# Optimization experiments

Measured on AMD Instinct MI355X. Metric: run time of the kernel, lower is better.

## Reference

```python
import jax, jax.numpy as jnp
import numpy as np


def setup_inputs() -> dict:
    key = jax.random.key(0)
    k1, k2 = jax.random.split(key)
    x = jax.random.normal(k1, (16, 128, 64, 64), dtype=jnp.float32)
    # weight layout: [out_channels, in_channels, kh, kw], kernel must be 3 for the
    # original Python-loop bounds to match the allocated output size
    weight = jax.random.normal(k2, (256, 128, 3, 3), dtype=jnp.float32) * 0.05
    return {"x": x, "weight": weight}


def reference(x, weight):
    # Stride-1 conv2d with symmetric zero padding=1 (forward ignores bias/stride/
    # dilation/groups in the original module).
    pad = 1
    out = jax.lax.conv_general_dilated(
        x, weight,
        window_strides=(1, 1),
        padding=[(pad, pad), (pad, pad)],
        dimension_numbers=("NCHW", "OIHW", "NCHW"),
    )
    return out
```

## Files before the change

### kernel.cpp

```cpp
#include <hip/hip_runtime.h>
#include <hip/hip_bf16.h>
#include <stdint.h>

typedef short bf16x8 __attribute__((ext_vector_type(8)));
typedef float f32x16 __attribute__((ext_vector_type(16)));

#define N_IMG 16
#define C_IN  128
#define H_IMG 64
#define W_IMG 64
#define K_OUT 256

#define XB_BYTES (16ull*66*66*128*2)
#define WB_BYTES (9ull*256*128*2)
#define WS_NEED  (XB_BYTES + WB_BYTES)

#define LDSX_BYTES (6*66*256)
#define WCH_BYTES  16384
#define LDS_TOTAL  (LDSX_BYTES + 3*WCH_BYTES)

__device__ __forceinline__ void gload16(void* lds, const void* g) {
    __builtin_amdgcn_global_load_lds(
        (const __attribute__((address_space(1))) void*)g,
        (__attribute__((address_space(3))) void*)lds, 16, 0, 0);
}

__device__ __forceinline__ uint32_t pack2(float a, float b) {
    __hip_bfloat16 ha = __float2bfloat16(a), hb = __float2bfloat16(b);
    return (uint32_t)*(uint16_t*)&ha | ((uint32_t)*(uint16_t*)&hb << 16);
}

__global__ __launch_bounds__(256)
void transform_fused_kernel(const float* __restrict__ x, const float* __restrict__ w,
                            __hip_bfloat16* __restrict__ xb, __hip_bfloat16* __restrict__ wb) {
    __shared__ __align__(16) uint32_t xs[64 * 64];
    const int b = blockIdx.x;
    const int t = threadIdx.x;

    if (b < 1056) {
        const int yt = b % 66;
        const int n  = b / 66;
        const bool interior = (yt >= 1 && yt <= 64);

        if (interior) {
            const float4* src = (const float4*)(x + (size_t)n * 524288 + (size_t)(yt - 1) * 64);
            #pragma unroll
            for (int it = 0; it < 4; ++it) {
                const int x4 = t & 15;
                const int j  = (t >> 4) + it * 16;
                float4 va = src[(2 * j) * 1024 + x4];
                float4 vb = src[(2 * j + 1) * 1024 + x4];
                const float* pa = (const float*)&va;
                const float* pb = (const float*)&vb;
                #pragma unroll
                for (int i = 0; i < 4; ++i) {
                    int row = x4 * 4 + i;
                    xs[row * 64 + (j ^ (((row >> 2) & 3) << 2))] = pack2(pa[i], pb[i]);
                }
            }
        }
        __syncthreads();

        uint4* dst = (uint4*)((char*)xb + (size_t)(n * 66 + yt) * 66 * 256);
        #pragma unroll
        for (int it = 0; it < 5; ++it) {
            int ch = t + it * 256;
            if (ch < 1056) {
                int xt = ch >> 4, u = ch & 15;
                uint4 val = make_uint4(0u, 0u, 0u, 0u);
                if (interior && xt >= 1 && xt <= 64) {
                    int row = xt - 1;
                    val = *(const uint4*)&xs[row * 64 + 4 * (u ^ ((row >> 2) & 3))];
                }
                dst[ch] = val;
            }
        }
    } else {
        const int kg = b - 1056;
        #pragma unroll
        for (int it = 0; it < 5; ++it) {
            int e = t + it * 256;
            if (e < 1152) {
                int tap = e >> 7;
                int c   = e & 127;
                wb[(tap * 256 + kg) * 128 + c] =
                    __float2bfloat16(w[kg * 1152 + c * 9 + tap]);
            }
        }
    }
}

__global__ __launch_bounds__(512, 2)
void conv3x3_mfma_kernel(const char* __restrict__ xg,
                         const char* __restrict__ wg,
                         float* __restrict__ out) {
    __shared__ uint4 smem[LDS_TOTAL / 16];
    char* lds  = (char*)smem;
    char* ldsW = lds + LDSX_BYTES;

    const int t    = threadIdx.x;
    const int b    = blockIdx.x;
    const int q    = b & 15;
    const int n    = b >> 4;
    const int lane = t & 63;
    const int wv   = t >> 6;
    const int lm   = lane & 31;
    const int hi   = lane >> 5;
    const int kb   = (wv >> 1) * 64;
    const int mb   = (wv & 1) * 128;

    int addrW[2][2];
    #pragma unroll
    for (int kf = 0; kf < 2; ++kf) {
        int krow = kb + kf * 32 + lm;
        #pragma unroll
        for (int ks = 0; ks < 2; ++ks)
            addrW[kf][ks] = krow * 64 + ((ks * 32 + hi * 16) ^ ((krow & 3) << 4));
    }
    int rc0[4];
    #pragma unroll
    for (int f = 0; f < 4; ++f) {
        int m = mb + f * 32 + lm;
        rc0[f] = (m >> 6) * 66 + (m & 63);
    }

    const int krow0 = t >> 2;
    const int woffA = krow0 * 256 + (((t & 3) ^ (krow0 & 3)) << 4);

    const char* xsrc = xg + (size_t)(n * 66 + q * 4) * 66 * 256;
    for (int ch = t; ch < 6336; ch += 512) {
        int L = ch * 16;
        gload16(lds + L, xsrc + (L ^ (((L >> 8) & 7) << 4)));
    }
    #pragma unroll
    for (int jj = 0; jj < 2; ++jj) {
        const char* s = wg + (jj >> 2) * 65536 + (jj & 3) * 64;
        char* d = ldsW + jj * WCH_BYTES + t * 16;
        gload16(d, s + woffA);
        gload16(d + 8192, s + woffA + 32768);
    }
    asm volatile("s_waitcnt vmcnt(2)" ::: "memory");
    __builtin_amdgcn_sched_barrier(0);
    __builtin_amdgcn_s_barrier();

    f32x16 acc[2][4];
    #pragma unroll
    for (int i = 0; i < 2; ++i)
        #pragma unroll
        for (int j = 0; j < 4; ++j)
            acc[i][j] = (f32x16)(0.f);

    int bR = 0;
    int bP = 2;

    auto loadx = [&](bf16x8 (&X)[2][4], int jj) {
        int tap = jj >> 2, cc = jj & 3;
        int r   = (tap >= 6) ? 2 : (tap >= 3 ? 1 : 0);
        int s_  = tap - r * 3;
        int rs66 = r * 66 + s_;
        #pragma unroll
        for (int ks = 0; ks < 2; ++ks) {
            const int co = cc * 64 + ks * 32 + hi * 16;
            #pragma unroll
            for (int f = 0; f < 4; ++f) {
                int rc = rc0[f] + rs66;
                int L  = rc * 256 + (co ^ ((rc & 7) << 4));
                X[ks][f] = *(const bf16x8*)(lds + L);
            }
        }
    };

    auto chunk = [&](int j, bf16x8 (&XC)[2][4], bf16x8 (&XN)[2][4]) {
        int jj2 = j + 2; if (jj2 >= 36) jj2 -= 36;
        {
            int tap2 = jj2 >> 2, cc2 = jj2 & 3;
            const char* s = wg + tap2 * 65536 + cc2 * 64;
            char* d = ldsW + bP * WCH_BYTES + t * 16;
            gload16(d, s + woffA);
            gload16(d + 8192, s + woffA + 32768);
        }
        const char* wbuf = ldsW + bR * WCH_BYTES;
        bf16x8 a[2][2];
        #pragma unroll
        for (int kf = 0; kf < 2; ++kf)
            #pragma unroll
            for (int ks = 0; ks < 2; ++ks)
                a[kf][ks] = *(const bf16x8*)(wbuf + addrW[kf][ks]);
        int jn = j + 1; if (jn >= 36) jn -= 36;
        loadx(XN, jn);

        __builtin_amdgcn_s_setprio(1);
        #pragma unroll
        for (int ks = 0; ks < 2; ++ks) {
            #pragma unroll
            for (int f = 0; f < 4; ++f) {
                acc[0][f] = __builtin_amdgcn_mfma_f32_32x32x16_bf16(a[0][ks], XC[ks][f], acc[0][f], 0, 0, 0);
                acc[1][f] = __builtin_amdgcn_mfma_f32_32x32x16_bf16(a[1][ks], XC[ks][f], acc[1][f], 0, 0, 0);
            }
        }
        __builtin_amdgcn_s_setprio(0);

        asm volatile("s_waitcnt vmcnt(2)" ::: "memory");
        __builtin_amdgcn_sched_barrier(0);
        __builtin_amdgcn_s_barrier();

        bR = (bR == 2) ? 0 : bR + 1;
        bP = (bP == 2) ? 0 : bP + 1;
    };

    bf16x8 xA[2][4], xB[2][4];
    loadx(xA, 0);
    for (int j = 0; j < 36; j += 2) {
        chunk(j,     xA, xB);
        chunk(j + 1, xB, xA);
    }

    const int y0 = q * 4;
    #pragma unroll
    for (int kf = 0; kf < 2; ++kf) {
        const int kbase2 = kb + kf * 32 + 4 * hi;
        #pragma unroll
        for (int f = 0; f < 4; ++f) {
            int m  = mb + f * 32 + lm;
            int yy = m >> 6;
            int xx = m & 63;
            float* op = out + (((size_t)(n * 256 + kbase2) * 64) + y0 + yy) * 64 + xx;
            #pragma unroll
            for (int reg = 0; reg < 16; ++reg) {
                int koff = (reg & 3) + 8 * (reg >> 2);
                op[(size_t)koff * 4096] = acc[kf][f][reg];
            }
        }
    }
}

__global__ __launch_bounds__(256, 3)
void conv3x3_f32_kernel(const float* __restrict__ x,
                        const float* __restrict__ w,
                        float* __restrict__ out) {
    __shared__ float xs[16][3][72];
    __shared__ float ws[16][9][64];

    const int t  = threadIdx.x;
    const int kt = blockIdx.x & 3;
    const int y  = (blockIdx.x >> 2) & 63;
    const int n  = blockIdx.x >> 8;

    const int k2   = t >> 3;
    const int xg   = t & 7;
    const int kloc = k2 * 2;
    const int x0   = xg * 8;

    float acc0[8] = {0.f,0.f,0.f,0.f,0.f,0.f,0.f,0.f};
    float acc1[8] = {0.f,0.f,0.f,0.f,0.f,0.f,0.f,0.f};

    const int k0 = kt * 64;

    for (int c0 = 0; c0 < C_IN; c0 += 16) {
        for (int idx = t; idx < 16 * 3 * 66; idx += 256) {
            int col = idx % 66;
            int rc  = idx / 66;
            int r   = rc % 3;
            int c   = rc / 3;
            int gx  = col - 1;
            int gy  = y - 1 + r;
            float v = 0.f;
            if ((unsigned)gx < (unsigned)W_IMG && (unsigned)gy < (unsigned)H_IMG)
                v = x[(((n * C_IN) + c0 + c) * H_IMG + gy) * W_IMG + gx];
            xs[c][r][col] = v;
        }
        for (int idx = t; idx < 64 * 16 * 9; idx += 256) {
            int tap = idx % 9;
            int ck  = idx / 9;
            int c   = ck % 16;
            int k   = ck / 16;
            ws[c][tap][k] = w[((k0 + k) * C_IN + c0 + c) * 9 + tap];
        }
        __syncthreads();

        #pragma unroll 2
        for (int c = 0; c < 16; ++c) {
            #pragma unroll
            for (int r = 0; r < 3; ++r) {
                float xr[10];
                #pragma unroll
                for (int i = 0; i < 10; ++i) xr[i] = xs[c][r][x0 + i];
                #pragma unroll
                for (int s = 0; s < 3; ++s) {
                    float w0 = ws[c][r * 3 + s][kloc];
                    float w1 = ws[c][r * 3 + s][kloc + 1];
                    #pragma unroll
                    for (int i = 0; i < 8; ++i) {
                        acc0[i] = fmaf(w0, xr[i + s], acc0[i]);
                        acc1[i] = fmaf(w1, xr[i + s], acc1[i]);
                    }
                }
            }
        }
        __syncthreads();
    }

    float* o0 = &out[(((n * K_OUT) + k0 + kloc) * H_IMG + y) * W_IMG + x0];
    float* o1 = o0 + H_IMG * W_IMG;
    #pragma unroll
    for (int i = 0; i < 8; ++i) o0[i] = acc0[i];
    #pragma unroll
    for (int i = 0; i < 8; ++i) o1[i] = acc1[i];
}

extern "C" void kernel_launch(void* const* d_in, const int* in_sizes, int n_in,
                              void* d_out, int out_size, void* d_ws, size_t ws_size,
                              hipStream_t stream) {
    const float* x = (const float*)d_in[0];
    const float* w = (const float*)d_in[1];
    float* out = (float*)d_out;
    (void)in_sizes; (void)n_in; (void)out_size;

    if (ws_size >= WS_NEED) {
        __hip_bfloat16* xb = (__hip_bfloat16*)d_ws;
        __hip_bfloat16* wb = (__hip_bfloat16*)((char*)d_ws + XB_BYTES);
        transform_fused_kernel<<<1056 + 256, 256, 0, stream>>>(x, w, xb, wb);
        conv3x3_mfma_kernel<<<256, 512, 0, stream>>>((const char*)xb, (const char*)wb, out);
    } else {
        conv3x3_f32_kernel<<<4096, 256, 0, stream>>>(x, w, out);
    }
}
```

Baseline: 132.9 us.

## Load conv weights directly from global into registers, drop LDS weight buffering

The weight transform now writes a pre-swizzled, MFMA-fragment-ordered layout, so each lane can load its A operands straight from global memory with contiguous 16-byte reads. The conv kernel drops the triple-buffered LDS weight staging and the per-chunk block barriers, and prefetches weight fragments two chunks ahead into registers. X fragment loads are restructured into a macro-unrolled per-tap loop with precomputed addresses. The aim is to remove LDS traffic and synchronization for weights, at the cost of more registers and exposing global/L2 latency on the weight loads.

After: 127.3 us. -4.2%, faster.

```diff
diff --git a/kernel.cpp b/kernel.cpp
--- a/kernel.cpp
+++ b/kernel.cpp
@@ -12,12 +12,10 @@
 #define K_OUT 256
 
 #define XB_BYTES (16ull*66*66*128*2)
-#define WB_BYTES (9ull*256*128*2)
+#define WB_BYTES (36ull*8*2*64*16)
 #define WS_NEED  (XB_BYTES + WB_BYTES)
 
 #define LDSX_BYTES (6*66*256)
-#define WCH_BYTES  16384
-#define LDS_TOTAL  (LDSX_BYTES + 3*WCH_BYTES)
 
 __device__ __forceinline__ void gload16(void* lds, const void* g) {
     __builtin_amdgcn_global_load_lds(
@@ -34,6 +32,7 @@
 void transform_fused_kernel(const float* __restrict__ x, const float* __restrict__ w,
                             __hip_bfloat16* __restrict__ xb, __hip_bfloat16* __restrict__ wb) {
     __shared__ __align__(16) uint32_t xs[64 * 64];
+    __shared__ float lw[1152];
     const int b = blockIdx.x;
     const int t = threadIdx.x;
 
@@ -77,26 +76,53 @@
         }
     } else {
         const int kg = b - 1056;
-        #pragma unroll
-        for (int it = 0; it < 5; ++it) {
-            int e = t + it * 256;
-            if (e < 1152) {
-                int tap = e >> 7;
-                int c   = e & 127;
-                wb[(tap * 256 + kg) * 128 + c] =
-                    __float2bfloat16(w[kg * 1152 + c * 9 + tap]);
-            }
-        }
-    }
-}
+        for (int e = t; e < 1152; e += 256) lw[e] = w[kg * 1152 + e];
+        __syncthreads();
+        const int basek = (kg >> 5) * 1024 + (kg & 31) * 8;
+        #pragma unroll
+        for (int tap = 0; tap < 9; ++tap) {
+            if (t < 128) {
+                int c = t;
+                int idx = (tap * 4 + (c >> 5)) * 8192 + basek
+                        + ((c >> 4) & 1) * 512 + ((c >> 3) & 1) * 256 + (c & 7);
+                wb[idx] = __float2bfloat16(lw[c * 9 + tap]);
+            }
+        }
+    }
+}
+
+#define CHUNK(CC, AU, XBN)                                                                    \
+  {                                                                                           \
+    _Pragma("unroll") for (int f = 0; f < 4; ++f)                         \
+      x1[f] = *(const bf16x8*)(lds + (xb0[f] ^ (((CC) << 6) | 32)));                          \
+    __builtin_amdgcn_s_setprio(1);                                                            \
+    _Pragma("unroll") for (int f = 0; f < 4; ++f) {                                           \
+      acc[0][f] = __builtin_amdgcn_mfma_f32_32x32x16_bf16(AU[0][0], x0[f], acc[0][f], 0, 0, 0); \
+      acc[1][f] = __builtin_amdgcn_mfma_f32_32x32x16_bf16(AU[1][0], x0[f], acc[1][f], 0, 0, 0); \
+    }                                                                                         \
+    __builtin_amdgcn_s_setprio(0);                                                            \
+    _Pragma("unroll") for (int f = 0; f < 4; ++f)                       \
+      x0[f] = *(const bf16x8*)(lds + ((XBN)[f] ^ ((((CC) + 1) & 3) << 6)));                   \
+    __builtin_amdgcn_s_setprio(1);                                                            \
+    _Pragma("unroll") for (int f = 0; f < 4; ++f) {                                           \
+      acc[0][f] = __builtin_amdgcn_mfma_f32_32x32x16_bf16(AU[0][1], x1[f], acc[0][f], 0, 0, 0); \
+      acc[1][f] = __builtin_amdgcn_mfma_f32_32x32x16_bf16(AU[1][1], x1[f], acc[1][f], 0, 0, 0); \
+    }                                                                                         \
+    __builtin_amdgcn_s_setprio(0);                                                            \
+    { int jj = tap * 4 + (CC) + 2; if (jj >= 36) jj -= 36;                  \
+      const char* wc = wgw + (size_t)jj * 16384;                                              \
+      _Pragma("unroll") for (int kf = 0; kf < 2; ++kf)                                        \
+        _Pragma("unroll") for (int ks = 0; ks < 2; ++ks)                                      \
+          AU[kf][ks] = *(const bf16x8*)(wc + kf * 2048 + ks * 1024);                          \
+    }                                                                                         \
+  }
 
 __global__ __launch_bounds__(512, 2)
 void conv3x3_mfma_kernel(const char* __restrict__ xg,
-                         const char* __restrict__ wg,
+                         const char* __restrict__ wg2,
                          float* __restrict__ out) {
-    __shared__ uint4 smem[LDS_TOTAL / 16];
-    char* lds  = (char*)smem;
-    char* ldsW = lds + LDSX_BYTES;
+    __shared__ uint4 smem[LDSX_BYTES / 16];
+    char* lds = (char*)smem;
 
     const int t    = threadIdx.x;
     const int b    = blockIdx.x;
@@ -108,40 +134,33 @@
     const int hi   = lane >> 5;
     const int kb   = (wv >> 1) * 64;
     const int mb   = (wv & 1) * 128;
-
-    int addrW[2][2];
-    #pragma unroll
-    for (int kf = 0; kf < 2; ++kf) {
-        int krow = kb + kf * 32 + lm;
-        #pragma unroll
-        for (int ks = 0; ks < 2; ++ks)
-            addrW[kf][ks] = krow * 64 + ((ks * 32 + hi * 16) ^ ((krow & 3) << 4));
-    }
+    const int hi4  = hi * 16;
+
     int rc0[4];
     #pragma unroll
     for (int f = 0; f < 4; ++f) {
         int m = mb + f * 32 + lm;
         rc0[f] = (m >> 6) * 66 + (m & 63);
     }
-
-    const int krow0 = t >> 2;
-    const int woffA = krow0 * 256 + (((t & 3) ^ (krow0 & 3)) << 4);
 
     const char* xsrc = xg + (size_t)(n * 66 + q * 4) * 66 * 256;
     for (int ch = t; ch < 6336; ch += 512) {
         int L = ch * 16;
         gload16(lds + L, xsrc + (L ^ (((L >> 8) & 7) << 4)));
     }
-    #pragma unroll
-    for (int jj = 0; jj < 2; ++jj) {
-        const char* s = wg + (jj >> 2) * 65536 + (jj & 3) * 64;
-        char* d = ldsW + jj * WCH_BYTES + t * 16;
-        gload16(d, s + woffA);
-        gload16(d + 8192, s + woffA + 32768);
-    }
-    asm volatile("s_waitcnt vmcnt(2)" ::: "memory");
-    __builtin_amdgcn_sched_barrier(0);
-    __builtin_amdgcn_s_barrier();
+
+    const char* wgw = wg2 + (wv >> 1) * 4096 + lane * 16;
+    bf16x8 aA[2][2], aB[2][2];
+    #pragma unroll
+    for (int kf = 0; kf < 2; ++kf)
+        #pragma unroll
+        for (int ks = 0; ks < 2; ++ks) {
+            aA[kf][ks] = *(const bf16x8*)(wgw + kf * 2048 + ks * 1024);
+            aB[kf][ks] = *(const bf16x8*)(wgw + 16384 + kf * 2048 + ks * 1024);
+        }
+
+    asm volatile("s_waitcnt vmcnt(0)" ::: "memory");
+    __syncthreads();
 
     f32x16 acc[2][4];
     #pragma unroll
@@ -150,69 +169,35 @@
         for (int j = 0; j < 4; ++j)
             acc[i][j] = (f32x16)(0.f);
 
-    int bR = 0;
-    int bP = 2;
-
-    auto loadx = [&](bf16x8 (&X)[2][4], int jj) {
-        int tap = jj >> 2, cc = jj & 3;
-        int r   = (tap >= 6) ? 2 : (tap >= 3 ? 1 : 0);
-        int s_  = tap - r * 3;
-        int rs66 = r * 66 + s_;
-        #pragma unroll
-        for (int ks = 0; ks < 2; ++ks) {
-            const int co = cc * 64 + ks * 32 + hi * 16;
+    int xb0[4], xbN[4];
+    #pragma unroll
+    for (int f = 0; f < 4; ++f) {
+        int rc = rc0[f];
+        xbN[f] = rc * 256 + (hi4 ^ ((rc & 7) << 4));
+    }
+
+    bf16x8 x0[4], x1[4];
+    #pragma unroll
+    for (int f = 0; f < 4; ++f)
+        x0[f] = *(const bf16x8*)(lds + xbN[f]);
+
+    for (int tap = 0; tap < 9; ++tap) {
+        #pragma unroll
+        for (int f = 0; f < 4; ++f) xb0[f] = xbN[f];
+        {
+            int tn = (tap < 8) ? tap + 1 : 8;
+            int rn = (tn >= 6) ? 2 : (tn >= 3 ? 1 : 0);
+            int rs = rn * 66 + (tn - rn * 3);
             #pragma unroll
             for (int f = 0; f < 4; ++f) {
-                int rc = rc0[f] + rs66;
-                int L  = rc * 256 + (co ^ ((rc & 7) << 4));
-                X[ks][f] = *(const bf16x8*)(lds + L);
-            }
-        }
-    };
-
-    auto chunk = [&](int j, bf16x8 (&XC)[2][4], bf16x8 (&XN)[2][4]) {
-        int jj2 = j + 2; if (jj2 >= 36) jj2 -= 36;
-        {
-            int tap2 = jj2 >> 2, cc2 = jj2 & 3;
-            const char* s = wg + tap2 * 65536 + cc2 * 64;
-            char* d = ldsW + bP * WCH_BYTES + t * 16;
-            gload16(d, s + woffA);
-            gload16(d + 8192, s + woffA + 32768);
-        }
-        const char* wbuf = ldsW + bR * WCH_BYTES;
-        bf16x8 a[2][2];
-        #pragma unroll
-        for (int kf = 0; kf < 2; ++kf)
-            #pragma unroll
-            for (int ks = 0; ks < 2; ++ks)
-                a[kf][ks] = *(const bf16x8*)(wbuf + addrW[kf][ks]);
-        int jn = j + 1; if (jn >= 36) jn -= 36;
-        loadx(XN, jn);
-
-        __builtin_amdgcn_s_setprio(1);
-        #pragma unroll
-        for (int ks = 0; ks < 2; ++ks) {
-            #pragma unroll
-            for (int f = 0; f < 4; ++f) {
-                acc[0][f] = __builtin_amdgcn_mfma_f32_32x32x16_bf16(a[0][ks], XC[ks][f], acc[0][f], 0, 0, 0);
-                acc[1][f] = __builtin_amdgcn_mfma_f32_32x32x16_bf16(a[1][ks], XC[ks][f], acc[1][f], 0, 0, 0);
-            }
-        }
-        __builtin_amdgcn_s_setprio(0);
-
-        asm volatile("s_waitcnt vmcnt(2)" ::: "memory");
-        __builtin_amdgcn_sched_barrier(0);
-        __builtin_amdgcn_s_barrier();
-
-        bR = (bR == 2) ? 0 : bR + 1;
-        bP = (bP == 2) ? 0 : bP + 1;
-    };
-
-    bf16x8 xA[2][4], xB[2][4];
-    loadx(xA, 0);
-    for (int j = 0; j < 36; j += 2) {
-        chunk(j,     xA, xB);
-        chunk(j + 1, xB, xA);
+                int rc = rc0[f] + rs;
+                xbN[f] = rc * 256 + (hi4 ^ ((rc & 7) << 4));
+            }
+        }
+        CHUNK(0, aA, xb0)
+        CHUNK(1, aB, xb0)
+        CHUNK(2, aA, xb0)
+        CHUNK(3, aB, xbN)
     }
 
     const int y0 = q * 4;
```
